# Optimization experiments

Hardware: AMD Instinct MI355X
Metric: run time of the kernel (lower is better)

Reference implementation:

```python
import jax, jax.numpy as jnp
import numpy as np
import math

B, C, H, W = 8, 256, 64, 64
KEYDIM, VALDIM = 128, 256


def conv3x3(x, w, b):
    # x: [B,C,H,W], w: [O,C,3,3] -> [B,O,H,W], SAME padding (padding=1)
    y = jax.lax.conv_general_dilated(x, w, window_strides=(1, 1), padding='SAME',
                                     dimension_numbers=('NCHW', 'OIHW', 'NCHW'))
    return y + b[None, :, None, None]


def setup_inputs() -> dict:
    key = jax.random.key(0)
    ks = jax.random.split(key, 5)
    x = jax.random.normal(ks[0], (B, C, H, W), dtype=jnp.float32)
    fan_in = C * 9
    s = 1.0 / np.sqrt(fan_in)
    key_w = jax.random.uniform(ks[1], (KEYDIM, C, 3, 3), jnp.float32, -s, s)
    key_b = jax.random.uniform(ks[2], (KEYDIM,), jnp.float32, -s, s)
    val_w = jax.random.uniform(ks[3], (VALDIM, C, 3, 3), jnp.float32, -s, s)
    val_b = jax.random.uniform(ks[4], (VALDIM,), jnp.float32, -s, s)
    return {"x": x, "key_w": key_w, "key_b": key_b, "val_w": val_w, "val_b": val_b}


def reference(x, key_w, key_b, val_w, val_b):
    b_, c_, h_, w_ = x.shape
    k = conv3x3(x, key_w, key_b).reshape(b_, KEYDIM, h_ * w_)   # [B,K,N]
    v = conv3x3(x, val_w, val_b)                                 # [B,V,H,W]
    sq = jnp.sum(k * k, axis=1)                                  # [B,N]
    a = sq[:, :, None]                                           # [B,N,1]
    c2 = sq[:, None, :]                                          # [B,1,N]
    dots = 2.0 * jnp.einsum('bki,bkj->bij', k, k)                # [B,N,N]
    affinity = (-a + dots - c2) / math.sqrt(KEYDIM)              # -||ki-kj||^2 / sqrt(K)
    affinity = jax.nn.softmax(affinity, axis=1)                  # softmax over dim=1 (rows)
    self_attn = jnp.einsum('bvi,bij->bvj', v.reshape(b_, VALDIM, h_ * w_), affinity)
    self_attn = self_attn.reshape(b_, VALDIM, h_, w_)
    return jnp.concatenate((v, self_attn), axis=1)               # [B,2V,H,W]
```

## Files before the change

### kernel.cpp

```cpp
#include <hip/hip_runtime.h>
#include <hip/hip_bf16.h>
#include <cstdint>

constexpr int Bb = 8, Cc = 256, Hh = 64, Ww = 64, Nn = 4096;
constexpr int KD = 128, VD = 256, HP = 66;

typedef __attribute__((ext_vector_type(8))) short short8_t;
typedef __attribute__((ext_vector_type(4))) short shortx4;
typedef __attribute__((ext_vector_type(4))) float floatx4;

constexpr float kScale = 0.08838834764831845f * 1.4426950408889634f;
constexpr float kTwoK  = 2.0f * kScale;

static __device__ __forceinline__ ushort f2bf(float f) {
    union { float f; uint32_t u; } v{f};
    uint32_t r = v.u + 0x7FFFu + ((v.u >> 16) & 1u);
    return (ushort)(r >> 16);
}
static __device__ __forceinline__ float bf2f(ushort b) {
    union { uint32_t u; float f; } v{(uint32_t)b << 16};
    return v.f;
}
static __device__ __forceinline__ uint32_t pk_bf16(float a, float b) {
    uint32_t r;
    asm("v_cvt_pk_bf16_f32 %0, %1, %2" : "=v"(r) : "v"(a), "v"(b));
    return r;
}
static __device__ __forceinline__ float exp2_raw(float x) {
    float r;
    asm("v_exp_f32 %0, %1" : "=v"(r) : "v"(x));
    return r;
}

static __device__ __forceinline__ void gload_lds16(const void* g, void* l) {
    __builtin_amdgcn_global_load_lds((const __attribute__((address_space(1))) uint32_t*)g,
                                     (__attribute__((address_space(3))) uint32_t*)l, 16, 0, 0);
}

__global__ __launch_bounds__(256) void pad_transpose(const float* __restrict__ x,
                                                     ushort* __restrict__ xpad) {
    int bid = blockIdx.x;
    int b = bid & 7, rest = bid >> 3;
    int y = rest & 63, cg = rest >> 6;
    int t = threadIdx.x;
    __shared__ float tile[64][65];
    int xcol = t & 63;
    int crow = t >> 6;
    const float* xb = x + ((size_t)(b * Cc + cg * 64) * Nn) + y * 64;
#pragma unroll
    for (int i = 0; i < 16; i++) {
        int c = crow + i * 4;
        tile[c][xcol] = xb[(size_t)c * Nn + xcol];
    }
    __syncthreads();
    int c = t & 63;
    int x4 = t >> 6;
    ushort* dst = xpad + (((size_t)(b * HP + (y + 1)) * HP) + 1) * Cc + cg * 64 + c;
#pragma unroll
    for (int i = 0; i < 16; i++) {
        int xx = x4 + i * 4;
        dst[(size_t)xx * Cc] = f2bf(tile[c][xx]);
    }
}

__global__ __launch_bounds__(256) void repack_w(const float* __restrict__ kw,
                                                const float* __restrict__ vw,
                                                ushort* __restrict__ wtk,
                                                ushort* __restrict__ wtv) {
    int idx = blockIdx.x * 256 + threadIdx.x;
    const int nk = KD * Cc;
    const int nv = VD * Cc;
    if (idx < nk) {
        const float* src = kw + (size_t)idx * 9;
        int oc = idx / Cc, c = idx % Cc;
#pragma unroll
        for (int r = 0; r < 9; r++) wtk[((size_t)r * KD + oc) * Cc + c] = f2bf(src[r]);
    } else if (idx < nk + nv) {
        int j = idx - nk;
        const float* src = vw + (size_t)j * 9;
        int oc = j / Cc, c = j % Cc;
#pragma unroll
        for (int r = 0; r < 9; r++) wtv[((size_t)r * VD + oc) * Cc + c] = f2bf(src[r]);
    }
}

template <int MODE, int OC>
__global__ __launch_bounds__(256) void conv_gemm(const ushort* __restrict__ xpad,
                                                 const ushort* __restrict__ wt,
                                                 const float* __restrict__ bias,
                                                 ushort* __restrict__ kt_out,
                                                 float* __restrict__ f32_out,
                                                 ushort* __restrict__ vb_out) {
    int bid = blockIdx.x;
    int b = bid & 7;
    int ocg, y;
    if (OC == 128) { ocg = 0; y = bid >> 3; }
    else           { ocg = (bid >> 3) & 1; y = bid >> 4; }
    int lane = threadIdx.x & 63, wv = threadIdx.x >> 6;
    int l15 = lane & 15, g = lane >> 4;
    int oc0 = ocg * 128;
    const int swzA = l15 & 7;

    __shared__ ushort wslab[2][128 * 128];

    size_t wsoff[8];
    int ldsrow[8];
#pragma unroll
    for (int h = 0; h < 8; h++) {
        int row = wv * 32 + h * 4 + (lane >> 4);
        wsoff[h] = (size_t)row * Cc + (((lane & 15) ^ (row & 7)) * 8);
        ldsrow[h] = (wv * 32 + h * 4) * 128;
    }

    floatx4 acc[8];
#pragma unroll
    for (int m = 0; m < 8; m++) acc[m] = (floatx4){0.f, 0.f, 0.f, 0.f};

    const ushort* xb = xpad + ((size_t)b * HP * HP) * Cc;
    int xcol = wv * 16 + l15;

    auto stage = [&](int hs, int bi) {
        int r = hs >> 1, hc = hs & 1;
        const ushort* wb = wt + ((size_t)r * OC + oc0) * Cc + hc * 128;
#pragma unroll
        for (int h = 0; h < 8; h++)
            gload_lds16(wb + wsoff[h], &wslab[bi][ldsrow[h]]);
    };

    stage(0, 0);
    __syncthreads();

#pragma unroll 1
    for (int hs = 0; hs < 18; ++hs) {
        int bi = hs & 1;
        if (hs < 17) stage(hs + 1, bi ^ 1);

        int r = hs >> 1, hc = hs & 1;
        int dy = r / 3, dx = r % 3;
        const ushort* bsrc = xb + ((size_t)(y + dy) * HP + xcol + dx) * Cc + hc * 128 + g * 8;
#pragma unroll
        for (int cc = 0; cc < 4; cc++) {
            short8_t bfrag = *(const short8_t*)(bsrc + cc * 32);
#pragma unroll
            for (int m = 0; m < 8; m++) {
                short8_t afrag = *(const short8_t*)&wslab[bi][(m * 16 + l15) * 128 + ((cc * 4 + g) ^ swzA) * 8];
                acc[m] = __builtin_amdgcn_mfma_f32_16x16x32_bf16(afrag, bfrag, acc[m], 0, 0, 0);
            }
        }
        __syncthreads();
    }

    int pos = y * 64 + xcol;
    if (MODE == 0) {
        ushort* kt = kt_out + ((size_t)(b * Nn + pos)) * KD;
#pragma unroll
        for (int m = 0; m < 8; m++) {
            floatx4 bv = *(const floatx4*)(bias + m * 16 + g * 4);
            shortx4 pk;
#pragma unroll
            for (int r = 0; r < 4; r++) pk[r] = (short)f2bf(acc[m][r] + bv[r]);
            *(shortx4*)(kt + m * 16 + g * 4) = pk;
        }
    } else {
#pragma unroll
        for (int m = 0; m < 8; m++) {
            floatx4 bv = *(const floatx4*)(bias + oc0 + m * 16 + g * 4);
#pragma unroll
            for (int r = 0; r < 4; r++) {
                int oc = oc0 + m * 16 + g * 4 + r;
                float v = acc[m][r] + bv[r];
                f32_out[((size_t)(b * 512 + oc)) * Nn + pos] = v;
                vb_out[((size_t)(b * VD + oc)) * Nn + pos] = f2bf(v);
            }
        }
    }
}

__global__ __launch_bounds__(256) void sq_kernel(const ushort* __restrict__ kt,
                                                 float* __restrict__ sq) {
    int bid = blockIdx.x;
    int idx = (bid & 7) * Nn + (bid >> 3) * 256 + threadIdx.x;
    const ushort* src = kt + (size_t)idx * KD;
    float s = 0.f;
#pragma unroll
    for (int i = 0; i < 16; i++) {
        short8_t v = *(const short8_t*)(src + i * 8);
#pragma unroll
        for (int e = 0; e < 8; e++) {
            float f = bf2f((ushort)v[e]);
            s += f * f;
        }
    }
    sq[idx] = s * kScale;
}

__global__ __launch_bounds__(256) void attn_kernel(const ushort* __restrict__ kt,
                                                   const ushort* __restrict__ vb,
                                                   const float* __restrict__ sq2,
                                                   float* __restrict__ out) {
    int bid = blockIdx.x;
    int b = bid & 7, jt = bid >> 3;
    int lane = threadIdx.x & 63, wv = threadIdx.x >> 6;
    int l15 = lane & 15, g = lane >> 4;

    __shared__ ushort bufK[64 * 128];
    __shared__ ushort bufV[256 * 64];
    __shared__ ushort pt[4][16][72];
    __shared__ float dls[4][16];

    const ushort* ktb = kt + ((size_t)b * Nn) * KD;
    const ushort* vbb = vb + ((size_t)b * VD) * Nn;
    const float* sqb = sq2 + b * Nn;

    const ushort* skp[4];
#pragma unroll
    for (int h = 0; h < 4; h++) {
        int row = wv * 16 + h * 4 + (lane >> 4);
        skp[h] = ktb + (size_t)row * KD + (((lane & 15) ^ (row & 7)) * 8);
    }
    const ushort* svp[8];
#pragma unroll
    for (int h = 0; h < 8; h++) {
        int vd = wv * 64 + h * 8 + (lane >> 3);
        svp[h] = vbb + (size_t)vd * Nn + (((lane & 7) ^ (vd & 7)) * 8);
    }

    int j = jt * 64 + wv * 16 + l15;
    short8_t kj[4];
#pragma unroll
    for (int kk = 0; kk < 4; kk++)
        kj[kk] = *(const short8_t*)(ktb + (size_t)j * KD + kk * 32 + g * 8);

    const int vh = wv >> 1, jh = wv & 1;

    floatx4 acc[8][2];
#pragma unroll
    for (int m = 0; m < 8; m++)
#pragma unroll
        for (int s = 0; s < 2; s++) acc[m][s] = (floatx4){0.f, 0.f, 0.f, 0.f};
    float dsum = 0.f;
    const int swzA = l15 & 7;

#pragma unroll
    for (int h = 0; h < 4; h++) gload_lds16(skp[h], &bufK[(wv * 16 + h * 4) * 128]);
#pragma unroll
    for (int h = 0; h < 8; h++) gload_lds16(svp[h], &bufV[(wv * 64 + h * 8) * 64]);
    __syncthreads();

#pragma unroll 1
    for (int it = 0; it < 64; ++it) {
        int i0 = it * 64;

        floatx4 sacc[4];
#pragma unroll
        for (int f = 0; f < 4; f++) sacc[f] = (floatx4){0.f, 0.f, 0.f, 0.f};
#pragma unroll
        for (int kk = 0; kk < 4; kk++) {
#pragma unroll
            for (int f = 0; f < 4; f++) {
                short8_t afr = *(const short8_t*)&bufK[(f * 16 + l15) * 128 + ((kk * 4 + g) ^ swzA) * 8];
                sacc[f] = __builtin_amdgcn_mfma_f32_16x16x32_bf16(afr, kj[kk], sacc[f], 0, 0, 0);
            }
        }
#pragma unroll
        for (int f = 0; f < 4; f++) {
            floatx4 sqi = *(const floatx4*)(sqb + i0 + f * 16 + g * 4);
            float p0 = exp2_raw(sacc[f][0] * kTwoK - sqi[0]);
            float p1 = exp2_raw(sacc[f][1] * kTwoK - sqi[1]);
            float p2 = exp2_raw(sacc[f][2] * kTwoK - sqi[2]);
            float p3 = exp2_raw(sacc[f][3] * kTwoK - sqi[3]);
            dsum += (p0 + p1) + (p2 + p3);
            uint2 w2 = {pk_bf16(p0, p1), pk_bf16(p2, p3)};
            *(uint2*)&pt[wv][l15][f * 16 + g * 4] = w2;
        }
        __syncthreads();

        if (it < 63) {
#pragma unroll
            for (int h = 0; h < 4; h++)
                gload_lds16(skp[h] + (size_t)(i0 + 64) * KD, &bufK[(wv * 16 + h * 4) * 128]);
        }

#pragma unroll
        for (int k2 = 0; k2 < 2; k2++) {
            short8_t pfr[2];
#pragma unroll
            for (int s = 0; s < 2; s++)
                pfr[s] = *(const short8_t*)&pt[jh * 2 + s][l15][k2 * 32 + g * 8];
#pragma unroll
            for (int m = 0; m < 8; m++) {
                int row = vh * 128 + m * 16 + l15;
                short8_t vfr = *(const short8_t*)&bufV[row * 64 + ((k2 * 4 + g) ^ swzA) * 8];
#pragma unroll
                for (int s = 0; s < 2; s++)
                    acc[m][s] = __builtin_amdgcn_mfma_f32_16x16x32_bf16(vfr, pfr[s], acc[m][s], 0, 0, 0);
            }
        }
        __syncthreads();

        if (it < 63) {
#pragma unroll
            for (int h = 0; h < 8; h++)
                gload_lds16(svp[h] + (i0 + 64), &bufV[(wv * 64 + h * 8) * 64]);
        }
    }

    dsum += __shfl_xor(dsum, 16, 64);
    dsum += __shfl_xor(dsum, 32, 64);
    if (g == 0) dls[wv][l15] = dsum;
    __syncthreads();
    float rden[2];
#pragma unroll
    for (int s = 0; s < 2; s++) rden[s] = 1.f / dls[jh * 2 + s][l15];

    float* ob = out + ((size_t)(b * 512 + 256 + vh * 128)) * Nn + jt * 64 + jh * 32 + l15;
#pragma unroll
    for (int m = 0; m < 8; m++) {
#pragma unroll
        for (int s = 0; s < 2; s++) {
#pragma unroll
            for (int r = 0; r < 4; r++) {
                int vd = m * 16 + g * 4 + r;
                ob[(size_t)vd * Nn + s * 16] = acc[m][s][r] * rden[s];
            }
        }
    }
}

extern "C" void kernel_launch(void* const* d_in, const int* in_sizes, int n_in,
                              void* d_out, int out_size, void* d_ws, size_t ws_size,
                              hipStream_t stream) {
    const float* x     = (const float*)d_in[0];
    const float* kw    = (const float*)d_in[1];
    const float* kbias = (const float*)d_in[2];
    const float* vw    = (const float*)d_in[3];
    const float* vbias = (const float*)d_in[4];
    float* out = (float*)d_out;
    char* ws = (char*)d_ws;

    constexpr size_t XPAD = 0;
    constexpr size_t WTK  = 17842176;
    constexpr size_t WTV  = 18432000;
    constexpr size_t KT   = 19611648;
    constexpr size_t VB   = 28000256;
    constexpr size_t SQ   = 44777472;

    ushort* xpad = (ushort*)(ws + XPAD);
    ushort* wtk  = (ushort*)(ws + WTK);
    ushort* wtv  = (ushort*)(ws + WTV);
    ushort* ktw  = (ushort*)(ws + KT);
    ushort* vbw  = (ushort*)(ws + VB);
    float*  sqw  = (float*)(ws + SQ);

    hipMemsetAsync(xpad, 0, 17842176, stream);
    pad_transpose<<<dim3(2048), 256, 0, stream>>>(x, xpad);
    repack_w<<<dim3(384), 256, 0, stream>>>(kw, vw, wtk, wtv);
    conv_gemm<0, KD><<<dim3(512), 256, 0, stream>>>(xpad, wtk, kbias, ktw, nullptr, nullptr);
    conv_gemm<1, VD><<<dim3(1024), 256, 0, stream>>>(xpad, wtv, vbias, nullptr, out, vbw);
    sq_kernel<<<dim3(128), 256, 0, stream>>>(ktw, sqw);
    attn_kernel<<<dim3(512), 256, 0, stream>>>(ktw, vbw, sqw, out);
}
```

Baseline: 249.3 us.

## Compute two output rows per conv block and split attention P tile in halves

The conv GEMM now computes two image rows per block, reusing each LDS weight fragment for two MFMAs and halving both the grid size and the number of weight-slab loads. The attention kernel splits the 64-column P tile into two 32-column halves, adding a barrier per half and shrinking the pt LDS buffer, and reuses that buffer for the denominator sums. These changes are meant to cut repeated weight traffic and shared-memory footprint, at the cost of more accumulator registers in the conv and extra synchronization in the attention loop.

```diff
diff --git a/kernel.cpp b/kernel.cpp
--- a/kernel.cpp
+++ b/kernel.cpp
@@ -93,9 +93,9 @@
                                                  ushort* __restrict__ vb_out) {
     int bid = blockIdx.x;
     int b = bid & 7;
-    int ocg, y;
-    if (OC == 128) { ocg = 0; y = bid >> 3; }
-    else           { ocg = (bid >> 3) & 1; y = bid >> 4; }
+    int ocg, y0;
+    if (OC == 128) { ocg = 0; y0 = (bid >> 3) * 2; }
+    else           { ocg = (bid >> 3) & 1; y0 = (bid >> 4) * 2; }
     int lane = threadIdx.x & 63, wv = threadIdx.x >> 6;
     int l15 = lane & 15, g = lane >> 4;
     int oc0 = ocg * 128;
@@ -112,9 +112,11 @@
         ldsrow[h] = (wv * 32 + h * 4) * 128;
     }
 
-    floatx4 acc[8];
-#pragma unroll
-    for (int m = 0; m < 8; m++) acc[m] = (floatx4){0.f, 0.f, 0.f, 0.f};
+    floatx4 acc[8][2];
+#pragma unroll
+    for (int m = 0; m < 8; m++)
+#pragma unroll
+        for (int rr = 0; rr < 2; rr++) acc[m][rr] = (floatx4){0.f, 0.f, 0.f, 0.f};
 
     const ushort* xb = xpad + ((size_t)b * HP * HP) * Cc;
     int xcol = wv * 16 + l15;
@@ -137,40 +139,46 @@
 
         int r = hs >> 1, hc = hs & 1;
         int dy = r / 3, dx = r % 3;
-        const ushort* bsrc = xb + ((size_t)(y + dy) * HP + xcol + dx) * Cc + hc * 128 + g * 8;
+        const ushort* bsrc0 = xb + ((size_t)(y0 + dy) * HP + xcol + dx) * Cc + hc * 128 + g * 8;
+        const ushort* bsrc1 = bsrc0 + (size_t)HP * Cc;
 #pragma unroll
         for (int cc = 0; cc < 4; cc++) {
-            short8_t bfrag = *(const short8_t*)(bsrc + cc * 32);
+            short8_t bfragA = *(const short8_t*)(bsrc0 + cc * 32);
+            short8_t bfragB = *(const short8_t*)(bsrc1 + cc * 32);
 #pragma unroll
             for (int m = 0; m < 8; m++) {
                 short8_t afrag = *(const short8_t*)&wslab[bi][(m * 16 + l15) * 128 + ((cc * 4 + g) ^ swzA) * 8];
-                acc[m] = __builtin_amdgcn_mfma_f32_16x16x32_bf16(afrag, bfrag, acc[m], 0, 0, 0);
-            }
-        }
-        __syncthreads();
-    }
-
-    int pos = y * 64 + xcol;
-    if (MODE == 0) {
-        ushort* kt = kt_out + ((size_t)(b * Nn + pos)) * KD;
-#pragma unroll
-        for (int m = 0; m < 8; m++) {
-            floatx4 bv = *(const floatx4*)(bias + m * 16 + g * 4);
-            shortx4 pk;
-#pragma unroll
-            for (int r = 0; r < 4; r++) pk[r] = (short)f2bf(acc[m][r] + bv[r]);
-            *(shortx4*)(kt + m * 16 + g * 4) = pk;
-        }
-    } else {
-#pragma unroll
-        for (int m = 0; m < 8; m++) {
-            floatx4 bv = *(const floatx4*)(bias + oc0 + m * 16 + g * 4);
-#pragma unroll
-            for (int r = 0; r < 4; r++) {
-                int oc = oc0 + m * 16 + g * 4 + r;
-                float v = acc[m][r] + bv[r];
-                f32_out[((size_t)(b * 512 + oc)) * Nn + pos] = v;
-                vb_out[((size_t)(b * VD + oc)) * Nn + pos] = f2bf(v);
+                acc[m][0] = __builtin_amdgcn_mfma_f32_16x16x32_bf16(afrag, bfragA, acc[m][0], 0, 0, 0);
+                acc[m][1] = __builtin_amdgcn_mfma_f32_16x16x32_bf16(afrag, bfragB, acc[m][1], 0, 0, 0);
+            }
+        }
+        __syncthreads();
+    }
+
+#pragma unroll
+    for (int rr = 0; rr < 2; rr++) {
+        int pos = (y0 + rr) * 64 + xcol;
+        if (MODE == 0) {
+            ushort* kt = kt_out + ((size_t)(b * Nn + pos)) * KD;
+#pragma unroll
+            for (int m = 0; m < 8; m++) {
+                floatx4 bv = *(const floatx4*)(bias + m * 16 + g * 4);
+                shortx4 pk;
+#pragma unroll
+                for (int r = 0; r < 4; r++) pk[r] = (short)f2bf(acc[m][rr][r] + bv[r]);
+                *(shortx4*)(kt + m * 16 + g * 4) = pk;
+            }
+        } else {
+#pragma unroll
+            for (int m = 0; m < 8; m++) {
+                floatx4 bv = *(const floatx4*)(bias + oc0 + m * 16 + g * 4);
+#pragma unroll
+                for (int r = 0; r < 4; r++) {
+                    int oc = oc0 + m * 16 + g * 4 + r;
+                    float v = acc[m][rr][r] + bv[r];
+                    f32_out[((size_t)(b * 512 + oc)) * Nn + pos] = v;
+                    vb_out[((size_t)(b * VD + oc)) * Nn + pos] = f2bf(v);
+                }
             }
         }
     }
@@ -205,8 +213,7 @@
 
     __shared__ ushort bufK[64 * 128];
     __shared__ ushort bufV[256 * 64];
-    __shared__ ushort pt[4][16][72];
-    __shared__ float dls[4][16];
+    __shared__ ushort pt[4][16][40];
 
     const ushort* ktb = kt + ((size_t)b * Nn) * KD;
     const ushort* vbb = vb + ((size_t)b * VD) * Nn;
@@ -263,7 +270,7 @@
             }
         }
 #pragma unroll
-        for (int f = 0; f < 4; f++) {
+        for (int f = 0; f < 2; f++) {
             floatx4 sqi = *(const floatx4*)(sqb + i0 + f * 16 + g * 4);
             float p0 = exp2_raw(sacc[f][0] * kTwoK - sqi[0]);
             float p1 = exp2_raw(sacc[f][1] * kTwoK - sqi[1]);
@@ -281,16 +288,15 @@
                 gload_lds16(skp[h] + (size_t)(i0 + 64) * KD, &bufK[(wv * 16 + h * 4) * 128]);
         }
 
-#pragma unroll
-        for (int k2 = 0; k2 < 2; k2++) {
+        {
             short8_t pfr[2];
 #pragma unroll
             for (int s = 0; s < 2; s++)
-                pfr[s] = *(const short8_t*)&pt[jh * 2 + s][l15][k2 * 32 + g * 8];
+                pfr[s] = *(const short8_t*)&pt[jh * 2 + s][l15][g * 8];
 #pragma unroll
             for (int m = 0; m < 8; m++) {
                 int row = vh * 128 + m * 16 + l15;
-                short8_t vfr = *(const short8_t*)&bufV[row * 64 + ((k2 * 4 + g) ^ swzA) * 8];
+                short8_t vfr = *(const short8_t*)&bufV[row * 64 + ((0 * 4 + g) ^ swzA) * 8];
 #pragma unroll
                 for (int s = 0; s < 2; s++)
                     acc[m][s] = __builtin_amdgcn_mfma_f32_16x16x32_bf16(vfr, pfr[s], acc[m][s], 0, 0, 0);
@@ -298,6 +304,35 @@
         }
         __syncthreads();
 
+#pragma unroll
+        for (int f = 2; f < 4; f++) {
+            floatx4 sqi = *(const floatx4*)(sqb + i0 + f * 16 + g * 4);
+            float p0 = exp2_raw(sacc[f][0] * kTwoK - sqi[0]);
+            float p1 = exp2_raw(sacc[f][1] * kTwoK - sqi[1]);
+            float p2 = exp2_raw(sacc[f][2] * kTwoK - sqi[2]);
+            float p3 = exp2_raw(sacc[f][3] * kTwoK - sqi[3]);
+            dsum += (p0 + p1) + (p2 + p3);
+            uint2 w2 = {pk_bf16(p0, p1), pk_bf16(p2, p3)};
+            *(uint2*)&pt[wv][l15][(f - 2) * 16 + g * 4] = w2;
+        }
+        __syncthreads();
+
+        {
+            short8_t pfr[2];
+#pragma unroll
+            for (int s = 0; s < 2; s++)
+                pfr[s] = *(const short8_t*)&pt[jh * 2 + s][l15][g * 8];
+#pragma unroll
+            for (int m = 0; m < 8; m++) {
+                int row = vh * 128 + m * 16 + l15;
+                short8_t vfr = *(const short8_t*)&bufV[row * 64 + ((1 * 4 + g) ^ swzA) * 8];
+#pragma unroll
+                for (int s = 0; s < 2; s++)
+                    acc[m][s] = __builtin_amdgcn_mfma_f32_16x16x32_bf16(vfr, pfr[s], acc[m][s], 0, 0, 0);
+            }
+        }
+        __syncthreads();
+
         if (it < 63) {
 #pragma unroll
             for (int h = 0; h < 8; h++)
@@ -307,11 +342,12 @@
 
     dsum += __shfl_xor(dsum, 16, 64);
     dsum += __shfl_xor(dsum, 32, 64);
-    if (g == 0) dls[wv][l15] = dsum;
+    float* dls = (float*)&pt[0][0][0];
+    if (g == 0) dls[wv * 16 + l15] = dsum;
     __syncthreads();
     float rden[2];
 #pragma unroll
-    for (int s = 0; s < 2; s++) rden[s] = 1.f / dls[jh * 2 + s][l15];
+    for (int s = 0; s < 2; s++) rden[s] = 1.f / dls[(jh * 2 + s) * 16 + l15];
 
     float* ob = out + ((size_t)(b * 512 + 256 + vh * 128)) * Nn + jt * 64 + jh * 32 + l15;
 #pragma unroll
@@ -355,8 +391,8 @@
     hipMemsetAsync(xpad, 0, 17842176, stream);
     pad_transpose<<<dim3(2048), 256, 0, stream>>>(x, xpad);
     repack_w<<<dim3(384), 256, 0, stream>>>(kw, vw, wtk, wtv);
-    conv_gemm<0, KD><<<dim3(512), 256, 0, stream>>>(xpad, wtk, kbias, ktw, nullptr, nullptr);
-    conv_gemm<1, VD><<<dim3(1024), 256, 0, stream>>>(xpad, wtv, vbias, nullptr, out, vbw);
+    conv_gemm<0, KD><<<dim3(256), 256, 0, stream>>>(xpad, wtk, kbias, ktw, nullptr, nullptr);
+    conv_gemm<1, VD><<<dim3(512), 256, 0, stream>>>(xpad, wtv, vbias, nullptr, out, vbw);
     sq_kernel<<<dim3(128), 256, 0, stream>>>(ktw, sqw);
     attn_kernel<<<dim3(512), 256, 0, stream>>>(ktw, vbw, sqw, out);
 }
```

New measurement: 266.0 us. 6.7% more time.

## Fuse squared-norm into key conv epilogue and compute two rows per value-conv block

Applied to the files above, without the earlier changes.

The separate sq_kernel launch is removed. Squared norms of the bf16-rounded keys are now computed in the key convolution epilogue with a cross-lane shuffle reduction. The value convolution now has each block compute two output rows, so each weight slab staged in LDS is reused across twice as many MFMAs and half as many blocks are launched. In exchange, accumulator registers double, which may lower occupancy, and the grid shrinks to 512 blocks.

```diff
diff --git a/kernel.cpp b/kernel.cpp
--- a/kernel.cpp
+++ b/kernel.cpp
@@ -84,18 +84,95 @@
     }
 }
 
-template <int MODE, int OC>
-__global__ __launch_bounds__(256) void conv_gemm(const ushort* __restrict__ xpad,
-                                                 const ushort* __restrict__ wt,
-                                                 const float* __restrict__ bias,
-                                                 ushort* __restrict__ kt_out,
-                                                 float* __restrict__ f32_out,
-                                                 ushort* __restrict__ vb_out) {
+__global__ __launch_bounds__(256) void conv_k(const ushort* __restrict__ xpad,
+                                              const ushort* __restrict__ wt,
+                                              const float* __restrict__ bias,
+                                              ushort* __restrict__ kt_out,
+                                              float* __restrict__ sq_out) {
+    int bid = blockIdx.x;
+    int b = bid & 7, y = bid >> 3;
+    int lane = threadIdx.x & 63, wv = threadIdx.x >> 6;
+    int l15 = lane & 15, g = lane >> 4;
+    const int swzA = l15 & 7;
+
+    __shared__ ushort wslab[2][128 * 128];
+
+    size_t wsoff[8];
+    int ldsrow[8];
+#pragma unroll
+    for (int h = 0; h < 8; h++) {
+        int row = wv * 32 + h * 4 + (lane >> 4);
+        wsoff[h] = (size_t)row * Cc + (((lane & 15) ^ (row & 7)) * 8);
+        ldsrow[h] = (wv * 32 + h * 4) * 128;
+    }
+
+    floatx4 acc[8];
+#pragma unroll
+    for (int m = 0; m < 8; m++) acc[m] = (floatx4){0.f, 0.f, 0.f, 0.f};
+
+    const ushort* xb = xpad + ((size_t)b * HP * HP) * Cc;
+    int xcol = wv * 16 + l15;
+
+    auto stage = [&](int hs, int bi) {
+        int r = hs >> 1, hc = hs & 1;
+        const ushort* wb = wt + ((size_t)r * KD) * Cc + hc * 128;
+#pragma unroll
+        for (int h = 0; h < 8; h++)
+            gload_lds16(wb + wsoff[h], &wslab[bi][ldsrow[h]]);
+    };
+
+    stage(0, 0);
+    __syncthreads();
+
+#pragma unroll 1
+    for (int hs = 0; hs < 18; ++hs) {
+        int bi = hs & 1;
+        if (hs < 17) stage(hs + 1, bi ^ 1);
+
+        int r = hs >> 1, hc = hs & 1;
+        int dy = r / 3, dx = r % 3;
+        const ushort* bsrc = xb + ((size_t)(y + dy) * HP + xcol + dx) * Cc + hc * 128 + g * 8;
+#pragma unroll
+        for (int cc = 0; cc < 4; cc++) {
+            short8_t bfrag = *(const short8_t*)(bsrc + cc * 32);
+#pragma unroll
+            for (int m = 0; m < 8; m++) {
+                short8_t afrag = *(const short8_t*)&wslab[bi][(m * 16 + l15) * 128 + ((cc * 4 + g) ^ swzA) * 8];
+                acc[m] = __builtin_amdgcn_mfma_f32_16x16x32_bf16(afrag, bfrag, acc[m], 0, 0, 0);
+            }
+        }
+        __syncthreads();
+    }
+
+    int pos = y * 64 + xcol;
+    ushort* kt = kt_out + ((size_t)(b * Nn + pos)) * KD;
+    float ssum = 0.f;
+#pragma unroll
+    for (int m = 0; m < 8; m++) {
+        floatx4 bv = *(const floatx4*)(bias + m * 16 + g * 4);
+        shortx4 pk;
+#pragma unroll
+        for (int r = 0; r < 4; r++) {
+            pk[r] = (short)f2bf(acc[m][r] + bv[r]);
+            float q = bf2f((ushort)pk[r]);
+            ssum += q * q;
+        }
+        *(shortx4*)(kt + m * 16 + g * 4) = pk;
+    }
+    ssum += __shfl_xor(ssum, 16, 64);
+    ssum += __shfl_xor(ssum, 32, 64);
+    if (g == 0) sq_out[b * Nn + pos] = ssum * kScale;
+}
+
+__global__ __launch_bounds__(256) void conv_v(const ushort* __restrict__ xpad,
+                                              const ushort* __restrict__ wt,
+                                              const float* __restrict__ bias,
+                                              float* __restrict__ f32_out,
+                                              ushort* __restrict__ vb_out) {
     int bid = blockIdx.x;
     int b = bid & 7;
-    int ocg, y;
-    if (OC == 128) { ocg = 0; y = bid >> 3; }
-    else           { ocg = (bid >> 3) & 1; y = bid >> 4; }
+    int ocg = (bid >> 3) & 1;
+    int y0 = (bid >> 4) * 2;
     int lane = threadIdx.x & 63, wv = threadIdx.x >> 6;
     int l15 = lane & 15, g = lane >> 4;
     int oc0 = ocg * 128;
@@ -112,16 +189,18 @@
         ldsrow[h] = (wv * 32 + h * 4) * 128;
     }
 
-    floatx4 acc[8];
-#pragma unroll
-    for (int m = 0; m < 8; m++) acc[m] = (floatx4){0.f, 0.f, 0.f, 0.f};
+    floatx4 acc[8][2];
+#pragma unroll
+    for (int m = 0; m < 8; m++)
+#pragma unroll
+        for (int rr = 0; rr < 2; rr++) acc[m][rr] = (floatx4){0.f, 0.f, 0.f, 0.f};
 
     const ushort* xb = xpad + ((size_t)b * HP * HP) * Cc;
     int xcol = wv * 16 + l15;
 
     auto stage = [&](int hs, int bi) {
         int r = hs >> 1, hc = hs & 1;
-        const ushort* wb = wt + ((size_t)r * OC + oc0) * Cc + hc * 128;
+        const ushort* wb = wt + ((size_t)r * VD + oc0) * Cc + hc * 128;
 #pragma unroll
         for (int h = 0; h < 8; h++)
             gload_lds16(wb + wsoff[h], &wslab[bi][ldsrow[h]]);
@@ -137,61 +216,37 @@
 
         int r = hs >> 1, hc = hs & 1;
         int dy = r / 3, dx = r % 3;
-        const ushort* bsrc = xb + ((size_t)(y + dy) * HP + xcol + dx) * Cc + hc * 128 + g * 8;
+        const ushort* bsrc0 = xb + ((size_t)(y0 + dy) * HP + xcol + dx) * Cc + hc * 128 + g * 8;
+        const ushort* bsrc1 = bsrc0 + (size_t)HP * Cc;
 #pragma unroll
         for (int cc = 0; cc < 4; cc++) {
-            short8_t bfrag = *(const short8_t*)(bsrc + cc * 32);
+            short8_t bfragA = *(const short8_t*)(bsrc0 + cc * 32);
+            short8_t bfragB = *(const short8_t*)(bsrc1 + cc * 32);
 #pragma unroll
             for (int m = 0; m < 8; m++) {
                 short8_t afrag = *(const short8_t*)&wslab[bi][(m * 16 + l15) * 128 + ((cc * 4 + g) ^ swzA) * 8];
-                acc[m] = __builtin_amdgcn_mfma_f32_16x16x32_bf16(afrag, bfrag, acc[m], 0, 0, 0);
+                acc[m][0] = __builtin_amdgcn_mfma_f32_16x16x32_bf16(afrag, bfragA, acc[m][0], 0, 0, 0);
+                acc[m][1] = __builtin_amdgcn_mfma_f32_16x16x32_bf16(afrag, bfragB, acc[m][1], 0, 0, 0);
             }
         }
         __syncthreads();
     }
 
-    int pos = y * 64 + xcol;
-    if (MODE == 0) {
-        ushort* kt = kt_out + ((size_t)(b * Nn + pos)) * KD;
-#pragma unroll
-        for (int m = 0; m < 8; m++) {
-            floatx4 bv = *(const floatx4*)(bias + m * 16 + g * 4);
-            shortx4 pk;
-#pragma unroll
-            for (int r = 0; r < 4; r++) pk[r] = (short)f2bf(acc[m][r] + bv[r]);
-            *(shortx4*)(kt + m * 16 + g * 4) = pk;
-        }
-    } else {
+#pragma unroll
+    for (int rr = 0; rr < 2; rr++) {
+        int pos = (y0 + rr) * 64 + xcol;
 #pragma unroll
         for (int m = 0; m < 8; m++) {
             floatx4 bv = *(const floatx4*)(bias + oc0 + m * 16 + g * 4);
 #pragma unroll
             for (int r = 0; r < 4; r++) {
                 int oc = oc0 + m * 16 + g * 4 + r;
-                float v = acc[m][r] + bv[r];
+                float v = acc[m][rr][r] + bv[r];
                 f32_out[((size_t)(b * 512 + oc)) * Nn + pos] = v;
                 vb_out[((size_t)(b * VD + oc)) * Nn + pos] = f2bf(v);
             }
         }
     }
-}
-
-__global__ __launch_bounds__(256) void sq_kernel(const ushort* __restrict__ kt,
-                                                 float* __restrict__ sq) {
-    int bid = blockIdx.x;
-    int idx = (bid & 7) * Nn + (bid >> 3) * 256 + threadIdx.x;
-    const ushort* src = kt + (size_t)idx * KD;
-    float s = 0.f;
-#pragma unroll
-    for (int i = 0; i < 16; i++) {
-        short8_t v = *(const short8_t*)(src + i * 8);
-#pragma unroll
-        for (int e = 0; e < 8; e++) {
-            float f = bf2f((ushort)v[e]);
-            s += f * f;
-        }
-    }
-    sq[idx] = s * kScale;
 }
 
 __global__ __launch_bounds__(256) void attn_kernel(const ushort* __restrict__ kt,
@@ -355,8 +410,7 @@
     hipMemsetAsync(xpad, 0, 17842176, stream);
     pad_transpose<<<dim3(2048), 256, 0, stream>>>(x, xpad);
     repack_w<<<dim3(384), 256, 0, stream>>>(kw, vw, wtk, wtv);
-    conv_gemm<0, KD><<<dim3(512), 256, 0, stream>>>(xpad, wtk, kbias, ktw, nullptr, nullptr);
-    conv_gemm<1, VD><<<dim3(1024), 256, 0, stream>>>(xpad, wtv, vbias, nullptr, out, vbw);
-    sq_kernel<<<dim3(128), 256, 0, stream>>>(ktw, sqw);
+    conv_k<<<dim3(512), 256, 0, stream>>>(xpad, wtk, kbias, ktw, sqw);
+    conv_v<<<dim3(512), 256, 0, stream>>>(xpad, wtv, vbias, out, vbw);
     attn_kernel<<<dim3(512), 256, 0, stream>>>(ktw, vbw, sqw, out);
 }
```

Result: no change. 247.5 us (-0.7%).
